# Kernel optimization log

Measured on AMD Instinct MI355X. Metric: run time of the kernel, lower is better.

## Reference

```python
import jax, jax.numpy as jnp
import numpy as np

EMBED_DIM = 1024
N_HEADS = 16
DK = EMBED_DIM // N_HEADS


def setup_inputs() -> dict:
    key = jax.random.key(0)
    ks = jax.random.split(key, 9)
    s = 1.0 / np.sqrt(EMBED_DIM)
    d = EMBED_DIM
    return {
        "x": jax.random.normal(ks[0], (2, 2048, d), dtype=jnp.float32),
        "Wq": jax.random.uniform(ks[1], (d, d), jnp.float32, -s, s),
        "bq": jax.random.uniform(ks[2], (d,), jnp.float32, -s, s),
        "Wk": jax.random.uniform(ks[3], (d, d), jnp.float32, -s, s),
        "bk": jax.random.uniform(ks[4], (d,), jnp.float32, -s, s),
        "Wv": jax.random.uniform(ks[5], (d, d), jnp.float32, -s, s),
        "bv": jax.random.uniform(ks[6], (d,), jnp.float32, -s, s),
        "Wo": jax.random.uniform(ks[7], (d, d), jnp.float32, -s, s),
        "bo": jax.random.uniform(ks[8], (d,), jnp.float32, -s, s),
    }


def reference(x, Wq, bq, Wk, bk, Wv, bv, Wo, bo):
    B, S, D = x.shape
    H, dk = N_HEADS, DK
    # QKV projections
    q = (x @ Wq + bq).reshape(B, S, H, dk).transpose(0, 2, 1, 3)  # [B,H,S,dk]
    k = (x @ Wk + bk).reshape(B, S, H, dk).transpose(0, 2, 1, 3)
    v = (x @ Wv + bv).reshape(B, S, H, dk).transpose(0, 2, 1, 3)
    # scaled dot-product attention with full score matrix (faithful to source)
    scores = jnp.einsum("bhqd,bhkd->bhqk", q, k) / jnp.sqrt(jnp.float32(dk))
    attn = jax.nn.softmax(scores, axis=-1)
    out = jnp.einsum("bhqk,bhkd->bhqd", attn, v)  # [B,H,S,dk]
    out = out.transpose(0, 2, 1, 3).reshape(B, S, D)
    return out @ Wo + bo
```

## Files before the change

kernel.cpp:

```cpp
#include <hip/hip_runtime.h>

typedef unsigned short u16;
typedef unsigned int u32;
typedef __attribute__((ext_vector_type(8))) short short8;
typedef __attribute__((ext_vector_type(4))) float float4v;

struct alignas(8) U16x4 { u16 x, y, z, w; };

__device__ __forceinline__ u16 f2b(float f) {
    union { float f; unsigned int u; } v; v.f = f;
    unsigned int r = (v.u >> 16) & 1u;
    v.u += 0x7fffu + r;
    return (u16)(v.u >> 16);
}

__device__ __forceinline__ float b2f(u16 u) {
    union { unsigned int u; float f; } v; v.u = ((u32)u) << 16; return v.f;
}

__device__ __forceinline__ void gld16(const u16* g, u16* l) {
    __builtin_amdgcn_global_load_lds(
        (const __attribute__((address_space(1))) void*)g,
        (__attribute__((address_space(3))) void*)l, 16, 0, 0);
}

__device__ __forceinline__ short8 frag8(const u16* base, int row, int cg) {
    return *(const short8*)(base + row * 64 + ((cg ^ (row & 7)) << 3));
}

__global__ __launch_bounds__(256) void prep_kernel(
    const float* __restrict__ x, const float* __restrict__ W0,
    const float* __restrict__ W1, const float* __restrict__ W2,
    const float* __restrict__ W3, u16* __restrict__ xb,
    u16* __restrict__ T0, u16* __restrict__ T1,
    u16* __restrict__ T2, u16* __restrict__ T3) {
    __shared__ float tile[32][33];
    int id = blockIdx.x;
    if (id < 4096) {
        size_t i = ((size_t)id * 256 + threadIdx.x) * 4;
        float4 v = *(const float4*)(x + i);
        U16x4 o;
        o.x = f2b(v.x); o.y = f2b(v.y); o.z = f2b(v.z); o.w = f2b(v.w);
        *(U16x4*)(xb + i) = o;
        return;
    }
    int r = id - 4096;
    int z = r >> 10, tl = r & 1023;
    const float* W = (z == 0) ? W0 : (z == 1) ? W1 : (z == 2) ? W2 : W3;
    u16* T = (z == 0) ? T0 : (z == 1) ? T1 : (z == 2) ? T2 : T3;
    int t = threadIdx.x;
    int tx = t & 31, ty = t >> 5;
    int bn = (tl & 31) * 32, bk = (tl >> 5) * 32;
#pragma unroll
    for (int p = 0; p < 4; ++p) {
        int k = ty + p * 8;
        tile[k][tx] = W[(size_t)(bk + k) * 1024 + bn + tx];
    }
    __syncthreads();
#pragma unroll
    for (int p = 0; p < 4; ++p) {
        int n = ty + p * 8;
        T[(size_t)(bn + n) * 1024 + bk + tx] = f2b(tile[tx][n]);
    }
}


__global__ __launch_bounds__(512, 2) void qkv_kernel(
    const u16* __restrict__ X,
    const u16* __restrict__ WqT, const u16* __restrict__ WkT, const u16* __restrict__ WvT,
    const float* __restrict__ bq, const float* __restrict__ bk, const float* __restrict__ bv,
    u16* __restrict__ Qo, u16* __restrict__ Ko, u16* __restrict__ VTo) {
    __shared__ __align__(16) u16 As[128 * 64];
    __shared__ __align__(16) u16 Bs[3][128 * 64];
    int id = blockIdx.x;
    int m = (id & 7) | (((id >> 3) & 3) << 3);
    int n = id >> 5;
    int t = threadIdx.x;
    int m0 = m * 128, n0 = n * 128;
    int lane = t & 63, wid = t >> 6;
    int wr = wid >> 2, wc = wid & 3;
    int l16 = lane & 15, quad = lane >> 4;
    int rl = lane >> 3, cs = lane & 7;

    int tileid = wid >> 1, half = wid & 1;
    const u16* gsrc = (tileid == 0) ? X : (tileid == 1) ? WqT
                     : (tileid == 2) ? WkT : WvT;
    int gbase = (tileid == 0) ? m0 : n0;
    u16* ldst = (tileid == 0) ? As : &Bs[tileid - 1][0];

    float4v acc[3][4][2];
    float4v zero4 = {0.f, 0.f, 0.f, 0.f};
#pragma unroll
    for (int z = 0; z < 3; ++z)
#pragma unroll
        for (int i = 0; i < 4; ++i)
#pragma unroll
            for (int j = 0; j < 2; ++j) acc[z][i][j] = zero4;

    for (int k0 = 0; k0 < 1024; k0 += 64) {
        __syncthreads();
#pragma unroll
        for (int p = 0; p < 8; ++p) {
            int q = half * 8 + p;
            int row = q * 8 + rl;
            int c = cs ^ (row & 7);
            gld16(gsrc + (size_t)(gbase + row) * 1024 + k0 + c * 8, ldst + q * 512);
        }
        __syncthreads();
#pragma unroll
        for (int ks = 0; ks < 64; ks += 32) {
            int cg = (ks >> 3) + quad;
            short8 af[4];
#pragma unroll
            for (int i = 0; i < 4; ++i)
                af[i] = frag8(As, wr * 64 + i * 16 + l16, cg);
#pragma unroll
            for (int z = 0; z < 3; ++z) {
                short8 bf[2];
#pragma unroll
                for (int j = 0; j < 2; ++j)
                    bf[j] = frag8(&Bs[z][0], wc * 32 + j * 16 + l16, cg);
#pragma unroll
                for (int i = 0; i < 4; ++i)
#pragma unroll
                    for (int j = 0; j < 2; ++j)
                        acc[z][i][j] = __builtin_amdgcn_mfma_f32_16x16x32_bf16(
                            af[i], bf[j], acc[z][i][j], 0, 0, 0);
            }
        }
    }

    const float QSCALE = 0.18033688011112042f;
#pragma unroll
    for (int j = 0; j < 2; ++j) {
        int n1 = n0 + wc * 32 + j * 16 + l16;
        float bql = bq[n1], bkl = bk[n1], bvl = bv[n1];
#pragma unroll
        for (int i = 0; i < 4; ++i) {
            int mbase = m0 + wr * 64 + i * 16 + quad * 4;
#pragma unroll
            for (int r = 0; r < 4; ++r) {
                Qo[(size_t)(mbase + r) * 1024 + n1] =
                    f2b((acc[0][i][j][r] + bql) * QSCALE);
                Ko[(size_t)(mbase + r) * 1024 + n1] =
                    f2b(acc[1][i][j][r] + bkl);
            }
            int bidx = mbase >> 11, s = mbase & 2047;
            size_t base =
                ((size_t)((bidx * 16 + (n1 >> 6)) * 64 + (n1 & 63))) * 2048 + s;
            U16x4 pk;
            pk.x = f2b(acc[2][i][j][0] + bvl);
            pk.y = f2b(acc[2][i][j][1] + bvl);
            pk.z = f2b(acc[2][i][j][2] + bvl);
            pk.w = f2b(acc[2][i][j][3] + bvl);
            *(U16x4*)(VTo + base) = pk;
        }
    }
}

__global__ __launch_bounds__(512) void oproj_kernel(const u16* __restrict__ X,
                                                    const u16* __restrict__ WoT,
                                                    const float* __restrict__ bias,
                                                    float* __restrict__ out) {
    __shared__ __align__(16) u16 As[128 * 64];
    __shared__ __align__(16) u16 Bs[128 * 64];
    int id = blockIdx.x;
    int m = (id & 7) | (((id >> 3) & 3) << 3);
    int n = id >> 5;
    int t = threadIdx.x;
    int m0 = m * 128, n0 = n * 128;
    int lane = t & 63, wid = t >> 6;
    int wr = wid >> 2, wc = wid & 3;
    int l16 = lane & 15, quad = lane >> 4;
    int rl = lane >> 3, cs = lane & 7;

    float4v acc[4][2];
    float4v zero4 = {0.f, 0.f, 0.f, 0.f};
#pragma unroll
    for (int i = 0; i < 4; ++i)
#pragma unroll
        for (int j = 0; j < 2; ++j) acc[i][j] = zero4;

    for (int k0 = 0; k0 < 1024; k0 += 64) {
        __syncthreads();
#pragma unroll
        for (int p = 0; p < 2; ++p) {
            int blk = wid * 2 + p;
            int row = blk * 8 + rl;
            int c = cs ^ (row & 7);
            gld16(X + (size_t)(m0 + row) * 1024 + k0 + c * 8, As + blk * 512);
            gld16(WoT + (size_t)(n0 + row) * 1024 + k0 + c * 8, Bs + blk * 512);
        }
        __syncthreads();
#pragma unroll
        for (int ks = 0; ks < 64; ks += 32) {
            int cg = (ks >> 3) + quad;
            short8 af[4], bf[2];
#pragma unroll
            for (int i = 0; i < 4; ++i) af[i] = frag8(As, wr * 64 + i * 16 + l16, cg);
#pragma unroll
            for (int j = 0; j < 2; ++j) bf[j] = frag8(Bs, wc * 32 + j * 16 + l16, cg);
#pragma unroll
            for (int i = 0; i < 4; ++i)
#pragma unroll
                for (int j = 0; j < 2; ++j)
                    acc[i][j] = __builtin_amdgcn_mfma_f32_16x16x32_bf16(
                        af[i], bf[j], acc[i][j], 0, 0, 0);
        }
    }

#pragma unroll
    for (int j = 0; j < 2; ++j) {
        int n1 = n0 + wc * 32 + j * 16 + l16;
        float bvl = bias[n1];
#pragma unroll
        for (int i = 0; i < 4; ++i) {
            int mbase = m0 + wr * 64 + i * 16 + quad * 4;
#pragma unroll
            for (int r = 0; r < 4; ++r)
                out[(size_t)(mbase + r) * 1024 + n1] = acc[i][j][r] + bvl;
        }
    }
}

__global__ __launch_bounds__(128, 2) void flash_kernel(const u16* __restrict__ Q,
                                                       const u16* __restrict__ Kn,
                                                       const u16* __restrict__ VT,
                                                       u16* __restrict__ Opart,
                                                       float* __restrict__ lpart) {
    __shared__ __align__(16) u16 Ks[64 * 64];
    __shared__ __align__(16) u16 Vs[64 * 64];
    __shared__ __align__(16) u16 Ps[128][72];

    int id = blockIdx.x;
    int bh = (id & 7) | (((id >> 3) & 3) << 3);
    int rest = id >> 5;
    int qb = rest & 15, kvz = rest >> 4;
    int b = bh >> 4, h = bh & 15;
    int t = threadIdx.x;
    int wid = t >> 6, lane = t & 63;
    int l16 = lane & 15, quad = lane >> 4;
    int rl = lane >> 3, cs = lane & 7;
    int q0 = qb * 128 + wid * 64;
    size_t kbase = (size_t)(b * 2048) * 1024 + h * 64;
    size_t vbase = (size_t)(bh * 64) * 2048;

    short8 qf[4][2];
#pragma unroll
    for (int j = 0; j < 4; ++j)
#pragma unroll
        for (int kk = 0; kk < 2; ++kk)
            qf[j][kk] = *(const short8*)(
                Q + ((size_t)(b * 2048 + q0 + j * 16 + l16)) * 1024 + h * 64 +
                kk * 32 + quad * 8);

    float4v oacc[4][4], lacc[4];
    float4v zero4 = {0.f, 0.f, 0.f, 0.f};
#pragma unroll
    for (int ip = 0; ip < 4; ++ip) {
        lacc[ip] = zero4;
#pragma unroll
        for (int jd = 0; jd < 4; ++jd) oacc[ip][jd] = zero4;
    }

    const short ONE = (short)0x3F80;
    short8 ones = {ONE, ONE, ONE, ONE, ONE, ONE, ONE, ONE};

    for (int kvi = 0; kvi < 16; ++kvi) {
        int kv = kvz * 1024 + kvi * 64;
        __syncthreads();
        if (wid == 0) {
#pragma unroll
            for (int p = 0; p < 8; ++p) {
                int row = p * 8 + rl;
                int c = cs ^ (row & 7);
                gld16(Kn + kbase + (size_t)(kv + row) * 1024 + c * 8, Ks + p * 512);
            }
        } else {
#pragma unroll
            for (int p = 0; p < 8; ++p) {
                int row = p * 8 + rl;
                int c = cs ^ (row & 7);
                gld16(VT + vbase + (size_t)row * 2048 + kv + c * 8, Vs + p * 512);
            }
        }
        __syncthreads();

#pragma unroll
        for (int i = 0; i < 4; ++i) {
            float4v sacc[4];
#pragma unroll
            for (int j = 0; j < 4; ++j) sacc[j] = zero4;
#pragma unroll
            for (int kk = 0; kk < 2; ++kk) {
                short8 kf = frag8(Ks, i * 16 + l16, kk * 4 + quad);
#pragma unroll
                for (int j = 0; j < 4; ++j)
                    sacc[j] = __builtin_amdgcn_mfma_f32_16x16x32_bf16(
                        kf, qf[j][kk], sacc[j], 0, 0, 0);
            }
#pragma unroll
            for (int j = 0; j < 4; ++j) {
                u32 e0 = __float_as_uint(__builtin_amdgcn_exp2f(sacc[j][0])) + 0x8000u;
                u32 e1 = __float_as_uint(__builtin_amdgcn_exp2f(sacc[j][1])) + 0x8000u;
                u32 e2 = __float_as_uint(__builtin_amdgcn_exp2f(sacc[j][2])) + 0x8000u;
                u32 e3 = __float_as_uint(__builtin_amdgcn_exp2f(sacc[j][3])) + 0x8000u;
                uint2 pk;
                pk.x = __builtin_amdgcn_perm(e1, e0, 0x07060302u);
                pk.y = __builtin_amdgcn_perm(e3, e2, 0x07060302u);
                *(uint2*)(&Ps[wid * 64 + j * 16 + l16][i * 16 + quad * 4]) = pk;
            }
        }

#pragma unroll
        for (int kk = 0; kk < 2; ++kk) {
            int cg = kk * 4 + quad;
            short8 pf[4];
#pragma unroll
            for (int ip = 0; ip < 4; ++ip)
                pf[ip] = *(const short8*)(
                    &Ps[wid * 64 + ip * 16 + l16][kk * 32 + quad * 8]);
#pragma unroll
            for (int jd = 0; jd < 4; ++jd) {
                short8 vf = frag8(Vs, jd * 16 + l16, cg);
#pragma unroll
                for (int ip = 0; ip < 4; ++ip)
                    oacc[ip][jd] = __builtin_amdgcn_mfma_f32_16x16x32_bf16(
                        pf[ip], vf, oacc[ip][jd], 0, 0, 0);
            }
#pragma unroll
            for (int ip = 0; ip < 4; ++ip)
                lacc[ip] = __builtin_amdgcn_mfma_f32_16x16x32_bf16(
                    pf[ip], ones, lacc[ip], 0, 0, 0);
        }
    }

    size_t obase = (size_t)kvz * 4194304;
#pragma unroll
    for (int ip = 0; ip < 4; ++ip)
#pragma unroll
        for (int r = 0; r < 4; ++r) {
            int q = q0 + ip * 16 + quad * 4 + r;
#pragma unroll
            for (int jd = 0; jd < 4; ++jd)
                Opart[obase + ((size_t)(b * 2048 + q)) * 1024 + h * 64 +
                      jd * 16 + l16] = f2b(oacc[ip][jd][r]);
        }
    if (l16 == 0) {
#pragma unroll
        for (int ip = 0; ip < 4; ++ip)
#pragma unroll
            for (int r = 0; r < 4; ++r) {
                int q = q0 + ip * 16 + quad * 4 + r;
                lpart[kvz * 65536 + (b * 2048 + q) * 16 + h] = lacc[ip][r];
            }
    }
}

__global__ __launch_bounds__(256) void combine_kernel(const u16* __restrict__ Op,
                                                      const float* __restrict__ lp,
                                                      u16* __restrict__ out) {
    int idx = blockIdx.x * 256 + threadIdx.x;
    size_t i = (size_t)idx * 4;
    int qg = idx >> 8;
    int d = (idx & 255) * 4;
    int h = d >> 6;
    float l0 = lp[qg * 16 + h], l1 = lp[65536 + qg * 16 + h];
    float inv = 1.0f / (l0 + l1);
    U16x4 o0 = *(const U16x4*)(Op + i);
    U16x4 o1 = *(const U16x4*)(Op + 4194304 + i);
    U16x4 o;
    o.x = f2b((b2f(o0.x) + b2f(o1.x)) * inv);
    o.y = f2b((b2f(o0.y) + b2f(o1.y)) * inv);
    o.z = f2b((b2f(o0.z) + b2f(o1.z)) * inv);
    o.w = f2b((b2f(o0.w) + b2f(o1.w)) * inv);
    *(U16x4*)(out + i) = o;
}

extern "C" void kernel_launch(void* const* d_in, const int* in_sizes, int n_in,
                              void* d_out, int out_size, void* d_ws, size_t ws_size,
                              hipStream_t stream) {
    const float* x  = (const float*)d_in[0];
    const float* Wq = (const float*)d_in[1];
    const float* bq = (const float*)d_in[2];
    const float* Wk = (const float*)d_in[3];
    const float* bk = (const float*)d_in[4];
    const float* Wv = (const float*)d_in[5];
    const float* bv = (const float*)d_in[6];
    const float* Wo = (const float*)d_in[7];
    const float* bo = (const float*)d_in[8];
    float* out = (float*)d_out;

    char* ws = (char*)d_ws;
    const size_t MB = 1024 * 1024;
    u16* xb  = (u16*)(ws);
    u16* wqt = (u16*)(ws + 8 * MB);
    u16* wkt = (u16*)(ws + 10 * MB);
    u16* wvt = (u16*)(ws + 12 * MB);
    u16* wot = (u16*)(ws + 14 * MB);
    u16* qb_ = (u16*)(ws + 16 * MB);
    u16* kb_ = (u16*)(ws + 24 * MB);
    u16* vt_ = (u16*)(ws + 32 * MB);
    u16* ab_ = (u16*)(ws + 40 * MB);
    u16* op_ = (u16*)(ws + 48 * MB);
    float* lp_ = (float*)(ws + 64 * MB);

    prep_kernel<<<8192, 256, 0, stream>>>(x, Wq, Wk, Wv, Wo, xb,
                                          wqt, wkt, wvt, wot);
    qkv_kernel<<<256, 512, 0, stream>>>(xb, wqt, wkt, wvt, bq, bk, bv,
                                        qb_, kb_, vt_);
    flash_kernel<<<1024, 128, 0, stream>>>(qb_, kb_, vt_, op_, lp_);
    combine_kernel<<<4096, 256, 0, stream>>>(op_, lp_, ab_);
    oproj_kernel<<<256, 512, 0, stream>>>(ab_, wot, bo, out);
}
```

Baseline: 192.9 us.

## Compute softmax row sums in registers and retile output projection to 64x128

The flash kernel stops computing the softmax denominator with extra MFMAs against a ones vector. It now accumulates the fp32 exp values per lane in registers and reduces them with cross-lane shuffles at the end, which cuts matrix-core work per KV tile. The sums now come from unrounded fp32 exps rather than the bf16-rounded P, a small numerical difference. Separately, the output projection uses 64x128 tiles with 256 threads and 512 blocks, giving more blocks on the GPU for this small GEMM at the cost of less operand reuse per block.

```diff
diff --git a/kernel.cpp b/kernel.cpp
--- a/kernel.cpp
+++ b/kernel.cpp
@@ -63,7 +63,6 @@
         T[(size_t)(bn + n) * 1024 + bk + tx] = f2b(tile[tx][n]);
     }
 }
-
 
 __global__ __launch_bounds__(512, 2) void qkv_kernel(
     const u16* __restrict__ X,
@@ -158,19 +157,18 @@
     }
 }
 
-__global__ __launch_bounds__(512) void oproj_kernel(const u16* __restrict__ X,
+__global__ __launch_bounds__(256) void oproj_kernel(const u16* __restrict__ X,
                                                     const u16* __restrict__ WoT,
                                                     const float* __restrict__ bias,
                                                     float* __restrict__ out) {
-    __shared__ __align__(16) u16 As[128 * 64];
+    __shared__ __align__(16) u16 As[64 * 64];
     __shared__ __align__(16) u16 Bs[128 * 64];
     int id = blockIdx.x;
-    int m = (id & 7) | (((id >> 3) & 3) << 3);
-    int n = id >> 5;
+    int m = (id & 7) | (((id >> 3) & 7) << 3);
+    int n = id >> 6;
     int t = threadIdx.x;
-    int m0 = m * 128, n0 = n * 128;
+    int m0 = m * 64, n0 = n * 128;
     int lane = t & 63, wid = t >> 6;
-    int wr = wid >> 2, wc = wid & 3;
     int l16 = lane & 15, quad = lane >> 4;
     int rl = lane >> 3, cs = lane & 7;
 
@@ -189,6 +187,12 @@
             int row = blk * 8 + rl;
             int c = cs ^ (row & 7);
             gld16(X + (size_t)(m0 + row) * 1024 + k0 + c * 8, As + blk * 512);
+        }
+#pragma unroll
+        for (int p = 0; p < 4; ++p) {
+            int blk = wid * 4 + p;
+            int row = blk * 8 + rl;
+            int c = cs ^ (row & 7);
             gld16(WoT + (size_t)(n0 + row) * 1024 + k0 + c * 8, Bs + blk * 512);
         }
         __syncthreads();
@@ -197,9 +201,9 @@
             int cg = (ks >> 3) + quad;
             short8 af[4], bf[2];
 #pragma unroll
-            for (int i = 0; i < 4; ++i) af[i] = frag8(As, wr * 64 + i * 16 + l16, cg);
-#pragma unroll
-            for (int j = 0; j < 2; ++j) bf[j] = frag8(Bs, wc * 32 + j * 16 + l16, cg);
+            for (int i = 0; i < 4; ++i) af[i] = frag8(As, i * 16 + l16, cg);
+#pragma unroll
+            for (int j = 0; j < 2; ++j) bf[j] = frag8(Bs, wid * 32 + j * 16 + l16, cg);
 #pragma unroll
             for (int i = 0; i < 4; ++i)
 #pragma unroll
@@ -211,11 +215,11 @@
 
 #pragma unroll
     for (int j = 0; j < 2; ++j) {
-        int n1 = n0 + wc * 32 + j * 16 + l16;
+        int n1 = n0 + wid * 32 + j * 16 + l16;
         float bvl = bias[n1];
 #pragma unroll
         for (int i = 0; i < 4; ++i) {
-            int mbase = m0 + wr * 64 + i * 16 + quad * 4;
+            int mbase = m0 + i * 16 + quad * 4;
 #pragma unroll
             for (int r = 0; r < 4; ++r)
                 out[(size_t)(mbase + r) * 1024 + n1] = acc[i][j][r] + bvl;
@@ -254,17 +258,15 @@
                 Q + ((size_t)(b * 2048 + q0 + j * 16 + l16)) * 1024 + h * 64 +
                 kk * 32 + quad * 8);
 
-    float4v oacc[4][4], lacc[4];
+    float4v oacc[4][4];
+    float lreg[4];
     float4v zero4 = {0.f, 0.f, 0.f, 0.f};
 #pragma unroll
     for (int ip = 0; ip < 4; ++ip) {
-        lacc[ip] = zero4;
+        lreg[ip] = 0.f;
 #pragma unroll
         for (int jd = 0; jd < 4; ++jd) oacc[ip][jd] = zero4;
     }
-
-    const short ONE = (short)0x3F80;
-    short8 ones = {ONE, ONE, ONE, ONE, ONE, ONE, ONE, ONE};
 
     for (int kvi = 0; kvi < 16; ++kvi) {
         int kv = kvz * 1024 + kvi * 64;
@@ -301,10 +303,15 @@
             }
 #pragma unroll
             for (int j = 0; j < 4; ++j) {
-                u32 e0 = __float_as_uint(__builtin_amdgcn_exp2f(sacc[j][0])) + 0x8000u;
-                u32 e1 = __float_as_uint(__builtin_amdgcn_exp2f(sacc[j][1])) + 0x8000u;
-                u32 e2 = __float_as_uint(__builtin_amdgcn_exp2f(sacc[j][2])) + 0x8000u;
-                u32 e3 = __float_as_uint(__builtin_amdgcn_exp2f(sacc[j][3])) + 0x8000u;
+                float e0f = __builtin_amdgcn_exp2f(sacc[j][0]);
+                float e1f = __builtin_amdgcn_exp2f(sacc[j][1]);
+                float e2f = __builtin_amdgcn_exp2f(sacc[j][2]);
+                float e3f = __builtin_amdgcn_exp2f(sacc[j][3]);
+                lreg[j] += (e0f + e1f) + (e2f + e3f);
+                u32 e0 = __float_as_uint(e0f) + 0x8000u;
+                u32 e1 = __float_as_uint(e1f) + 0x8000u;
+                u32 e2 = __float_as_uint(e2f) + 0x8000u;
+                u32 e3 = __float_as_uint(e3f) + 0x8000u;
                 uint2 pk;
                 pk.x = __builtin_amdgcn_perm(e1, e0, 0x07060302u);
                 pk.y = __builtin_amdgcn_perm(e3, e2, 0x07060302u);
@@ -328,11 +335,13 @@
                     oacc[ip][jd] = __builtin_amdgcn_mfma_f32_16x16x32_bf16(
                         pf[ip], vf, oacc[ip][jd], 0, 0, 0);
             }
-#pragma unroll
-            for (int ip = 0; ip < 4; ++ip)
-                lacc[ip] = __builtin_amdgcn_mfma_f32_16x16x32_bf16(
-                    pf[ip], ones, lacc[ip], 0, 0, 0);
-        }
+        }
+    }
+
+#pragma unroll
+    for (int j = 0; j < 4; ++j) {
+        lreg[j] += __shfl_xor(lreg[j], 16);
+        lreg[j] += __shfl_xor(lreg[j], 32);
     }
 
     size_t obase = (size_t)kvz * 4194304;
@@ -346,14 +355,12 @@
                 Opart[obase + ((size_t)(b * 2048 + q)) * 1024 + h * 64 +
                       jd * 16 + l16] = f2b(oacc[ip][jd][r]);
         }
-    if (l16 == 0) {
-#pragma unroll
-        for (int ip = 0; ip < 4; ++ip)
-#pragma unroll
-            for (int r = 0; r < 4; ++r) {
-                int q = q0 + ip * 16 + quad * 4 + r;
-                lpart[kvz * 65536 + (b * 2048 + q) * 16 + h] = lacc[ip][r];
-            }
+    if (quad == 0) {
+#pragma unroll
+        for (int j = 0; j < 4; ++j) {
+            int q = q0 + j * 16 + l16;
+            lpart[kvz * 65536 + (b * 2048 + q) * 16 + h] = lreg[j];
+        }
     }
 }
 
@@ -411,5 +418,5 @@
                                         qb_, kb_, vt_);
     flash_kernel<<<1024, 128, 0, stream>>>(qb_, kb_, vt_, op_, lp_);
     combine_kernel<<<4096, 256, 0, stream>>>(op_, lp_, ab_);
-    oproj_kernel<<<256, 512, 0, stream>>>(ab_, wot, bo, out);
-}
+    oproj_kernel<<<512, 256, 0, stream>>>(ab_, wot, bo, out);
+}
```

After: 192.0 us. No clear change (-0.4%).
